# Optimization experiments

Measured on AMD Instinct MI355X. Metric: run time of the kernel, lower is better.

## Reference

```python
import jax, jax.numpy as jnp
import numpy as np

N_NODES = 50000
N_EDGES = 400000
IN_CH = 109
OUT_CH = 32


def setup_inputs() -> dict:
    key = jax.random.key(0)
    ks = jax.random.split(key, 12)
    dims = [(IN_CH, 10 * OUT_CH), (10 * OUT_CH, 2 * OUT_CH), (2 * OUT_CH, OUT_CH), (2 * OUT_CH, OUT_CH)]
    inp = {
        'x': jax.random.normal(ks[0], (N_NODES, IN_CH), dtype=jnp.float32),
        'edge_index': jax.random.randint(ks[1], (2, N_EDGES), 0, N_NODES, dtype=jnp.int64) if jax.config.jax_enable_x64 else jax.random.randint(ks[1], (2, N_EDGES), 0, N_NODES, dtype=jnp.int32),
    }
    names = ['W1', 'b1', 'W2', 'b2', 'Wmu', 'bmu', 'Wls', 'bls']
    for i, (fi, fo) in enumerate(dims):
        scale = 1.0 / np.sqrt(fi)
        inp[names[2 * i]] = jax.random.uniform(ks[2 + 2 * i], (fi, fo), minval=-scale, maxval=scale, dtype=jnp.float32)
        inp[names[2 * i + 1]] = jnp.zeros((fo,), dtype=jnp.float32)
    return inp


def _gcn_conv(x, src, dst, norm, W, b, n):
    # PyG GCNConv: h = x @ W, then symmetric-normalized aggregation, then + b
    h = x @ W                                   # [N, F_out]
    msg = h[src] * norm[:, None]                # [E+N, F_out]
    out = jax.ops.segment_sum(msg, dst, num_segments=n)
    return out + b


def _norm_and_loops(edge_index, n):
    # add self loops, compute D^{-1/2}(A+I)D^{-1/2} edge weights
    loops = jnp.arange(n, dtype=edge_index.dtype)
    src = jnp.concatenate([edge_index[0], loops])
    dst = jnp.concatenate([edge_index[1], loops])
    deg = jax.ops.segment_sum(jnp.ones_like(src, dtype=jnp.float32), dst, num_segments=n)
    dinv = jnp.where(deg > 0, jax.lax.rsqrt(jnp.maximum(deg, 1.0)), 0.0)
    norm = dinv[src] * dinv[dst]
    return src, dst, norm


def reference(x, edge_index, W1, b1, W2, b2, Wmu, bmu, Wls, bls):
    n = x.shape[0]
    src, dst, norm = _norm_and_loops(edge_index, n)
    h = jax.nn.relu(_gcn_conv(x, src, dst, norm, W1, b1, n))
    h = jax.nn.relu(_gcn_conv(h, src, dst, norm, W2, b2, n))
    mu = _gcn_conv(h, src, dst, norm, Wmu, bmu, n)
    logstd = _gcn_conv(h, src, dst, norm, Wls, bls, n)
    return (mu, logstd)
```

## Files before the change

kernel.cpp:

```cpp
#include <hip/hip_runtime.h>

#define NN 50000
#define NE 400000

typedef __attribute__((ext_vector_type(8))) short short8v;
typedef __attribute__((ext_vector_type(4))) float f32x4;

__device__ __forceinline__ unsigned short f2bf_rtn(float x) {
    unsigned u = __float_as_uint(x);
    unsigned r = u + 0x7FFFu + ((u >> 16) & 1u);
    return (unsigned short)(r >> 16);
}
__device__ __forceinline__ float bf2f(unsigned short h) {
    return __uint_as_float(((unsigned)h) << 16);
}

__global__ void prep_kernel(const float* __restrict__ x,
                            const float* __restrict__ W1, const float* __restrict__ W2,
                            const float* __restrict__ Wmu, const float* __restrict__ Wls,
                            unsigned* __restrict__ xp, int* __restrict__ zero_base,
                            unsigned short* __restrict__ w1t_hi,
                            unsigned short* __restrict__ w2t_hi,
                            unsigned short* __restrict__ wct_hi) {
    int b = blockIdx.x, tid = threadIdx.x;
    if (b < 12500) {
        int idx = b * 256 + tid;
        int i = idx >> 6, c2 = (idx & 63) * 2;
        long xb = (long)i * 109;
        float v0 = (c2 < 109) ? x[xb + c2] : 0.0f;
        float v1 = (c2 + 1 < 109) ? x[xb + c2 + 1] : 0.0f;
        xp[idx] = (unsigned)f2bf_rtn(v0) | ((unsigned)f2bf_rtn(v1) << 16);
    } else if (b < 12891) {
        int i = (b - 12500) * 256 + tid;
        if (i < 100096) zero_base[i] = 0;
    } else if (b < 13051) {
        int idx = (b - 12891) * 256 + tid;
        int n = idx >> 7, k = idx & 127;
        float v = (k < 109) ? W1[(long)k * 320 + n] : 0.0f;
        w1t_hi[idx] = f2bf_rtn(v);
    } else if (b < 13131) {
        int idx = (b - 13051) * 256 + tid;
        int n = idx / 320, k = idx - n * 320;
        w2t_hi[idx] = f2bf_rtn(W2[(long)k * 64 + n]);
    } else {
        int idx = (b - 13131) * 256 + tid;
        int n = idx >> 6, k = idx & 63;
        float v = (n < 32) ? Wmu[k * 32 + n] : Wls[k * 32 + (n - 32)];
        wct_hi[idx] = f2bf_rtn(v);
    }
}

__global__ void hist_kernel(const int* __restrict__ dst, int* __restrict__ counts) {
    for (int e = blockIdx.x * blockDim.x + threadIdx.x; e < NE; e += gridDim.x * blockDim.x)
        atomicAdd(&counts[dst[e]], 1);
}

__global__ void dinv_scan1_kernel(const int* __restrict__ counts, float* __restrict__ dinv,
                                  int* __restrict__ rowstart, int* __restrict__ bsum) {
    __shared__ int tmp[256];
    int tid = threadIdx.x;
    int i = blockIdx.x * 256 + tid;
    int v = (i < NN) ? counts[i] : 0;
    if (i < NN) dinv[i] = rsqrtf((float)(v + 1));
    tmp[tid] = v;
    __syncthreads();
    for (int off = 1; off < 256; off <<= 1) {
        int t = 0;
        if (tid >= off) t = tmp[tid - off];
        __syncthreads();
        if (tid >= off) tmp[tid] += t;
        __syncthreads();
    }
    if (i < NN) rowstart[i] = tmp[tid] - v;
    if (tid == 255) bsum[blockIdx.x] = tmp[255];
}

__global__ void scan23_kernel(int* __restrict__ rowstart, const int* __restrict__ bsum) {
    __shared__ int red[4];
    int tid = threadIdx.x;
    int v = (tid < 196 && tid < (int)blockIdx.x) ? bsum[tid] : 0;
    for (int off = 32; off > 0; off >>= 1) v += __shfl_down(v, off, 64);
    if ((tid & 63) == 0) red[tid >> 6] = v;
    __syncthreads();
    int pref = red[0] + red[1] + red[2] + red[3];
    int i = blockIdx.x * 256 + tid;
    if (i < NN) rowstart[i] += pref;
    if (i == 0) rowstart[NN] = NE;
}

__global__ void scatter_kernel(const int* __restrict__ src, const int* __restrict__ dst,
                               const int* __restrict__ rowstart, int* __restrict__ cursor,
                               int* __restrict__ esrc) {
    for (int e = blockIdx.x * blockDim.x + threadIdx.x; e < NE; e += gridDim.x * blockDim.x) {
        int d = dst[e];
        int pos = rowstart[d] + atomicAdd(&cursor[d], 1);
        esrc[pos] = src[e];
    }
}

__global__ __launch_bounds__(256) void agg109_packed_kernel(const int* __restrict__ rowstart,
                                                            const int* __restrict__ esrc,
                                                            const float* __restrict__ dinv,
                                                            const unsigned* __restrict__ xp,
                                                            unsigned* __restrict__ xa_hi32) {
    int wave = blockIdx.x * (blockDim.x >> 6) + (threadIdx.x >> 6);
    if (wave >= NN) return;
    int lane = threadIdx.x & 63;
    float wd = dinv[wave];
    unsigned pself = xp[(long)wave * 64 + lane];
    float acc0 = __uint_as_float(pself << 16) * wd;
    float acc1 = __uint_as_float(pself & 0xFFFF0000u) * wd;
    int j0 = rowstart[wave], j1 = rowstart[wave + 1];
    int j = j0;
    for (; j + 8 <= j1; j += 8) {
        int s[8];
        float w[8];
        unsigned pp[8];
        #pragma unroll
        for (int u = 0; u < 8; ++u) s[u] = esrc[j + u];
        #pragma unroll
        for (int u = 0; u < 8; ++u) w[u] = dinv[s[u]];
        #pragma unroll
        for (int u = 0; u < 8; ++u) pp[u] = xp[(long)s[u] * 64 + lane];
        #pragma unroll
        for (int u = 0; u < 8; ++u) {
            acc0 = fmaf(__uint_as_float(pp[u] << 16), w[u], acc0);
            acc1 = fmaf(__uint_as_float(pp[u] & 0xFFFF0000u), w[u], acc1);
        }
    }
    for (; j + 4 <= j1; j += 4) {
        int s0 = esrc[j], s1 = esrc[j + 1], s2 = esrc[j + 2], s3 = esrc[j + 3];
        float w0 = dinv[s0], w1 = dinv[s1], w2 = dinv[s2], w3 = dinv[s3];
        unsigned p0 = xp[(long)s0 * 64 + lane], p1 = xp[(long)s1 * 64 + lane];
        unsigned p2 = xp[(long)s2 * 64 + lane], p3 = xp[(long)s3 * 64 + lane];
        acc0 = fmaf(__uint_as_float(p0 << 16), w0, acc0);
        acc1 = fmaf(__uint_as_float(p0 & 0xFFFF0000u), w0, acc1);
        acc0 = fmaf(__uint_as_float(p1 << 16), w1, acc0);
        acc1 = fmaf(__uint_as_float(p1 & 0xFFFF0000u), w1, acc1);
        acc0 = fmaf(__uint_as_float(p2 << 16), w2, acc0);
        acc1 = fmaf(__uint_as_float(p2 & 0xFFFF0000u), w2, acc1);
        acc0 = fmaf(__uint_as_float(p3 << 16), w3, acc0);
        acc1 = fmaf(__uint_as_float(p3 & 0xFFFF0000u), w3, acc1);
    }
    for (; j < j1; ++j) {
        int s = esrc[j];
        float w = dinv[s];
        unsigned pv = xp[(long)s * 64 + lane];
        acc0 = fmaf(__uint_as_float(pv << 16), w, acc0);
        acc1 = fmaf(__uint_as_float(pv & 0xFFFF0000u), w, acc1);
    }
    acc0 *= wd;
    acc1 *= wd;
    xa_hi32[(long)wave * 64 + lane] =
        (unsigned)f2bf_rtn(acc0) | ((unsigned)f2bf_rtn(acc1) << 16);
}

__global__ __launch_bounds__(256) void agg64_relu_bf16_kernel(const int* __restrict__ rowstart,
                                                              const int* __restrict__ esrc,
                                                              const float* __restrict__ dinv,
                                                              const unsigned short* __restrict__ g,
                                                              const float* __restrict__ b,
                                                              unsigned short* __restrict__ hhi) {
    int wave = blockIdx.x * (blockDim.x >> 6) + (threadIdx.x >> 6);
    if (wave >= NN) return;
    int lane = threadIdx.x & 63;
    long base = (long)wave * 64;
    float acc = bf2f(g[base + lane]);
    int j0 = rowstart[wave], j1 = rowstart[wave + 1];
    int j = j0;
    for (; j + 8 <= j1; j += 8) {
        int s[8];
        float pp[8];
        #pragma unroll
        for (int u = 0; u < 8; ++u) s[u] = esrc[j + u];
        #pragma unroll
        for (int u = 0; u < 8; ++u) pp[u] = bf2f(g[(long)s[u] * 64 + lane]);
        #pragma unroll
        for (int u = 0; u < 8; ++u) acc += pp[u];
    }
    for (; j + 4 <= j1; j += 4) {
        int s0 = esrc[j], s1 = esrc[j + 1], s2 = esrc[j + 2], s3 = esrc[j + 3];
        float p0 = bf2f(g[(long)s0 * 64 + lane]), p1 = bf2f(g[(long)s1 * 64 + lane]);
        float p2 = bf2f(g[(long)s2 * 64 + lane]), p3 = bf2f(g[(long)s3 * 64 + lane]);
        acc += p0 + p1 + p2 + p3;
    }
    for (; j < j1; ++j) acc += bf2f(g[(long)esrc[j] * 64 + lane]);
    float v = acc * dinv[wave] + b[lane];
    v = v > 0.0f ? v : 0.0f;
    hhi[base + lane] = f2bf_rtn(v);
}

__global__ __launch_bounds__(256) void agg64b_kernel(const int* __restrict__ rowstart,
                                                     const int* __restrict__ esrc,
                                                     const float* __restrict__ dinv,
                                                     const unsigned short* __restrict__ h,
                                                     unsigned short* __restrict__ a_hi) {
    int wave = blockIdx.x * (blockDim.x >> 6) + (threadIdx.x >> 6);
    if (wave >= NN) return;
    int lane = threadIdx.x & 63;
    long base = (long)wave * 64;
    float wd = dinv[wave];
    float acc = bf2f(h[base + lane]) * wd;
    int j0 = rowstart[wave], j1 = rowstart[wave + 1];
    int j = j0;
    for (; j + 8 <= j1; j += 8) {
        int s[8];
        float w[8], pp[8];
        #pragma unroll
        for (int u = 0; u < 8; ++u) s[u] = esrc[j + u];
        #pragma unroll
        for (int u = 0; u < 8; ++u) w[u] = dinv[s[u]];
        #pragma unroll
        for (int u = 0; u < 8; ++u) pp[u] = bf2f(h[(long)s[u] * 64 + lane]);
        #pragma unroll
        for (int u = 0; u < 8; ++u) acc = fmaf(pp[u], w[u], acc);
    }
    for (; j + 4 <= j1; j += 4) {
        int s0 = esrc[j], s1 = esrc[j + 1], s2 = esrc[j + 2], s3 = esrc[j + 3];
        float w0 = dinv[s0], w1 = dinv[s1], w2 = dinv[s2], w3 = dinv[s3];
        float p0 = bf2f(h[(long)s0 * 64 + lane]), p1 = bf2f(h[(long)s1 * 64 + lane]);
        float p2 = bf2f(h[(long)s2 * 64 + lane]), p3 = bf2f(h[(long)s3 * 64 + lane]);
        acc = fmaf(p0, w0, acc); acc = fmaf(p1, w1, acc);
        acc = fmaf(p2, w2, acc); acc = fmaf(p3, w3, acc);
    }
    for (; j < j1; ++j) {
        int s = esrc[j];
        acc = fmaf(bf2f(h[(long)s * 64 + lane]), dinv[s], acc);
    }
    a_hi[base + lane] = f2bf_rtn(acc * wd);
}

#define LDT 72

template <int MODE>
__global__ __launch_bounds__(256) void mfma_gemm_kernel(
    const unsigned short* __restrict__ Ahi,
    const unsigned short* __restrict__ Bhi,
    const float* __restrict__ bias, const float* __restrict__ bias2,
    const float* __restrict__ dinv,
    unsigned short* __restrict__ Chi,
    float* __restrict__ Cf, int M, int N, int K, int grid_n) {
    __shared__ unsigned short As[64 * LDT];
    __shared__ unsigned short Bs[64 * LDT];
    int tid = threadIdx.x;
    int wid = tid >> 6, lane = tid & 63;
    int l15 = lane & 15, l4 = lane >> 4;

    int T = gridDim.x;
    int xcd = blockIdx.x & 7, jj = blockIdx.x >> 3;
    int q = T >> 3, r = T & 7;
    int start = (xcd < r) ? xcd * (q + 1) : r * (q + 1) + (xcd - r) * q;
    int lin = start + jj;
    int bm = lin / grid_n, bn = lin - bm * grid_n;
    int bm0 = bm * 64, bn0 = bn * 64;

    f32x4 acc[4] = {};

    for (int kc = 0; kc < K; kc += 64) {
        #pragma unroll
        for (int r2 = 0; r2 < 2; ++r2) {
            int idx = tid + 256 * r2;
            int row = idx >> 3, slot = idx & 7;
            int grow = bm0 + row;
            if (grow >= M) grow = M - 1;
            long go = (long)grow * K + kc + slot * 8;
            *(uint4*)&As[row * LDT + slot * 8] = *(const uint4*)&Ahi[go];
            long gob = (long)(bn0 + row) * K + kc + slot * 8;
            *(uint4*)&Bs[row * LDT + slot * 8] = *(const uint4*)&Bhi[gob];
        }
        __syncthreads();
        #pragma unroll
        for (int ks = 0; ks < 2; ++ks) {
            int koff = ks * 32 + l4 * 8;
            int ra = (wid * 16 + l15) * LDT + koff;
            short8v ah = *(const short8v*)&As[ra];
            #pragma unroll
            for (int n = 0; n < 4; ++n) {
                int rb = (n * 16 + l15) * LDT + koff;
                short8v bh = *(const short8v*)&Bs[rb];
                acc[n] = __builtin_amdgcn_mfma_f32_16x16x32_bf16(ah, bh, acc[n], 0, 0, 0);
            }
        }
        __syncthreads();
    }
    int rbase = bm0 + wid * 16 + l4 * 4;
    #pragma unroll
    for (int q2 = 0; q2 < 4; ++q2) {
        int grow = rbase + q2;
        if (grow >= M) continue;
        float rs = (MODE == 1) ? dinv[grow] : 0.0f;
        #pragma unroll
        for (int n = 0; n < 4; ++n) {
            int gcol = bn0 + n * 16 + l15;
            float v = acc[n][q2];
            if (MODE == 0) {
                v += bias[gcol];
                v = v > 0.0f ? v : 0.0f;
                Chi[(long)grow * N + gcol] = f2bf_rtn(v);
            } else if (MODE == 1) {
                Chi[(long)grow * N + gcol] = f2bf_rtn(v * rs);
            } else {
                if (gcol < 32)
                    Cf[(long)grow * 32 + gcol] = v + bias[gcol];
                else
                    Cf[(long)NN * 32 + (long)grow * 32 + (gcol - 32)] = v + bias2[gcol - 32];
            }
        }
    }
}

extern "C" void kernel_launch(void* const* d_in, const int* in_sizes, int n_in,
                              void* d_out, int out_size, void* d_ws, size_t ws_size,
                              hipStream_t stream) {
    const float* x   = (const float*)d_in[0];
    const int*   ei  = (const int*)d_in[1];
    const int*   src = ei;
    const int*   dst = ei + NE;
    const float* W1  = (const float*)d_in[2];
    const float* b1  = (const float*)d_in[3];
    const float* W2  = (const float*)d_in[4];
    const float* b2  = (const float*)d_in[5];
    const float* Wmu = (const float*)d_in[6];
    const float* bmu = (const float*)d_in[7];
    const float* Wls = (const float*)d_in[8];
    const float* bls = (const float*)d_in[9];
    float* out = (float*)d_out;

    char* p = (char*)d_ws;
    float* dinv   = (float*)p; p += 50048 * 4;
    int* counts   = (int*)p;   p += 50048 * 4;
    int* cursor   = (int*)p;   p += 50048 * 4;
    int* rowstart = (int*)p;   p += 50056 * 4;
    int* bsum     = (int*)p;   p += 256 * 4;
    int* esrc     = (int*)p;   p += 400000 * 4;
    unsigned* xp          = (unsigned*)p;       p += 50000L * 64 * 4;
    unsigned short* xa_hi = (unsigned short*)p; p += 50000L * 128 * 2;
    unsigned short* a2_hi = (unsigned short*)p; p += 50000L * 64 * 2;
    unsigned short* g2b   = (unsigned short*)p; p += 50000L * 64 * 2;
    unsigned short* h1_hi = (unsigned short*)p; p += 50000L * 320 * 2;
    unsigned short* w1t_hi = (unsigned short*)p; p += 320 * 128 * 2;
    unsigned short* w2t_hi = (unsigned short*)p; p += 64 * 320 * 2;
    unsigned short* wct_hi = (unsigned short*)p; p += 64 * 64 * 2;
    unsigned short* h2_hi = xa_hi;

    const int TB = 256;
    const int NB_NODES = (NN + TB - 1) / TB;
    const int NB_AGG = (NN * 64 + TB - 1) / TB;

    prep_kernel<<<13147, TB, 0, stream>>>(x, W1, W2, Wmu, Wls, xp, counts,
                                          w1t_hi, w2t_hi, wct_hi);
    hist_kernel<<<1024, TB, 0, stream>>>(dst, counts);
    dinv_scan1_kernel<<<NB_NODES, TB, 0, stream>>>(counts, dinv, rowstart, bsum);
    scan23_kernel<<<NB_NODES, TB, 0, stream>>>(rowstart, bsum);
    scatter_kernel<<<1024, TB, 0, stream>>>(src, dst, rowstart, cursor, esrc);

    agg109_packed_kernel<<<NB_AGG, TB, 0, stream>>>(rowstart, esrc, dinv, xp,
                                                    (unsigned*)xa_hi);
    mfma_gemm_kernel<0><<<782 * 5, 256, 0, stream>>>(xa_hi, w1t_hi, b1, nullptr,
                                                     nullptr, h1_hi, nullptr,
                                                     NN, 320, 128, 5);

    mfma_gemm_kernel<1><<<782, 256, 0, stream>>>(h1_hi, w2t_hi, nullptr, nullptr,
                                                 dinv, g2b, nullptr,
                                                 NN, 64, 320, 1);
    agg64_relu_bf16_kernel<<<NB_AGG, TB, 0, stream>>>(rowstart, esrc, dinv, g2b, b2, h2_hi);

    agg64b_kernel<<<NB_AGG, TB, 0, stream>>>(rowstart, esrc, dinv, h2_hi, a2_hi);
    mfma_gemm_kernel<3><<<782, 256, 0, stream>>>(a2_hi, wct_hi, bmu, bls,
                                                 nullptr, nullptr, out,
                                                 NN, 64, 64, 1);
}
```

Before: 169.5 us.

## Fuse final aggregation with output GEMM into single LDS-staged kernel

Merges the last sparse aggregation (agg64b) and the 64x64 output GEMM into one kernel. Each 1024-thread block aggregates 64 nodes into shared memory as bf16, then 16 waves run MFMA against the staged weight tile and write mu/logstd directly. This removes one kernel launch and the global round trip of the 50000x64 intermediate. In exchange each wave handles four nodes serially, and the large block size may lower occupancy and latency hiding for the gather.

```diff
diff --git a/kernel.cpp b/kernel.cpp
--- a/kernel.cpp
+++ b/kernel.cpp
@@ -190,56 +190,94 @@
     hhi[base + lane] = f2bf_rtn(v);
 }
 
-__global__ __launch_bounds__(256) void agg64b_kernel(const int* __restrict__ rowstart,
-                                                     const int* __restrict__ esrc,
-                                                     const float* __restrict__ dinv,
-                                                     const unsigned short* __restrict__ h,
-                                                     unsigned short* __restrict__ a_hi) {
-    int wave = blockIdx.x * (blockDim.x >> 6) + (threadIdx.x >> 6);
-    if (wave >= NN) return;
-    int lane = threadIdx.x & 63;
-    long base = (long)wave * 64;
-    float wd = dinv[wave];
-    float acc = bf2f(h[base + lane]) * wd;
-    int j0 = rowstart[wave], j1 = rowstart[wave + 1];
-    int j = j0;
-    for (; j + 8 <= j1; j += 8) {
-        int s[8];
-        float w[8], pp[8];
-        #pragma unroll
-        for (int u = 0; u < 8; ++u) s[u] = esrc[j + u];
-        #pragma unroll
-        for (int u = 0; u < 8; ++u) w[u] = dinv[s[u]];
-        #pragma unroll
-        for (int u = 0; u < 8; ++u) pp[u] = bf2f(h[(long)s[u] * 64 + lane]);
-        #pragma unroll
-        for (int u = 0; u < 8; ++u) acc = fmaf(pp[u], w[u], acc);
-    }
-    for (; j + 4 <= j1; j += 4) {
-        int s0 = esrc[j], s1 = esrc[j + 1], s2 = esrc[j + 2], s3 = esrc[j + 3];
-        float w0 = dinv[s0], w1 = dinv[s1], w2 = dinv[s2], w3 = dinv[s3];
-        float p0 = bf2f(h[(long)s0 * 64 + lane]), p1 = bf2f(h[(long)s1 * 64 + lane]);
-        float p2 = bf2f(h[(long)s2 * 64 + lane]), p3 = bf2f(h[(long)s3 * 64 + lane]);
-        acc = fmaf(p0, w0, acc); acc = fmaf(p1, w1, acc);
-        acc = fmaf(p2, w2, acc); acc = fmaf(p3, w3, acc);
-    }
-    for (; j < j1; ++j) {
-        int s = esrc[j];
-        acc = fmaf(bf2f(h[(long)s * 64 + lane]), dinv[s], acc);
-    }
-    a_hi[base + lane] = f2bf_rtn(acc * wd);
-}
-
 #define LDT 72
+__global__ __launch_bounds__(1024) void agg_gemm3_kernel(const int* __restrict__ rowstart,
+                                                         const int* __restrict__ esrc,
+                                                         const float* __restrict__ dinv,
+                                                         const unsigned short* __restrict__ h,
+                                                         const unsigned short* __restrict__ wct_hi,
+                                                         const float* __restrict__ bmu,
+                                                         const float* __restrict__ bls,
+                                                         float* __restrict__ out) {
+    __shared__ unsigned short As[64 * LDT];
+    __shared__ unsigned short Bs[64 * LDT];
+    int tid = threadIdx.x;
+    int wid = tid >> 6, lane = tid & 63;
+    int m0 = blockIdx.x * 64;
+
+    if (tid < 512) {
+        int row = tid >> 3, slot = tid & 7;
+        *(uint4*)&Bs[row * LDT + slot * 8] = *(const uint4*)&wct_hi[row * 64 + slot * 8];
+    }
+
+    #pragma unroll
+    for (int t = 0; t < 4; ++t) {
+        int node = m0 + wid * 4 + t;
+        int i = node < NN ? node : NN - 1;
+        long base = (long)i * 64;
+        float wd = dinv[i];
+        float acc = bf2f(h[base + lane]) * wd;
+        int j0 = rowstart[i], j1 = rowstart[i + 1];
+        int j = j0;
+        for (; j + 8 <= j1; j += 8) {
+            int s[8];
+            float w[8], pp[8];
+            #pragma unroll
+            for (int u = 0; u < 8; ++u) s[u] = esrc[j + u];
+            #pragma unroll
+            for (int u = 0; u < 8; ++u) w[u] = dinv[s[u]];
+            #pragma unroll
+            for (int u = 0; u < 8; ++u) pp[u] = bf2f(h[(long)s[u] * 64 + lane]);
+            #pragma unroll
+            for (int u = 0; u < 8; ++u) acc = fmaf(pp[u], w[u], acc);
+        }
+        for (; j + 4 <= j1; j += 4) {
+            int s0 = esrc[j], s1 = esrc[j + 1], s2 = esrc[j + 2], s3 = esrc[j + 3];
+            float w0 = dinv[s0], w1 = dinv[s1], w2 = dinv[s2], w3 = dinv[s3];
+            float p0 = bf2f(h[(long)s0 * 64 + lane]), p1 = bf2f(h[(long)s1 * 64 + lane]);
+            float p2 = bf2f(h[(long)s2 * 64 + lane]), p3 = bf2f(h[(long)s3 * 64 + lane]);
+            acc = fmaf(p0, w0, acc); acc = fmaf(p1, w1, acc);
+            acc = fmaf(p2, w2, acc); acc = fmaf(p3, w3, acc);
+        }
+        for (; j < j1; ++j) {
+            int s = esrc[j];
+            acc = fmaf(bf2f(h[(long)s * 64 + lane]), dinv[s], acc);
+        }
+        As[(wid * 4 + t) * LDT + lane] = f2bf_rtn(acc * wd);
+    }
+    __syncthreads();
+
+    int r = wid >> 2, c = wid & 3;
+    int l15 = lane & 15, l4 = lane >> 4;
+    f32x4 acc4 = {};
+    #pragma unroll
+    for (int ks = 0; ks < 2; ++ks) {
+        int koff = ks * 32 + l4 * 8;
+        short8v ah = *(const short8v*)&As[(r * 16 + l15) * LDT + koff];
+        short8v bh = *(const short8v*)&Bs[(c * 16 + l15) * LDT + koff];
+        acc4 = __builtin_amdgcn_mfma_f32_16x16x32_bf16(ah, bh, acc4, 0, 0, 0);
+    }
+    int rbase = m0 + r * 16 + l4 * 4;
+    int gcol = c * 16 + l15;
+    #pragma unroll
+    for (int q2 = 0; q2 < 4; ++q2) {
+        int grow = rbase + q2;
+        if (grow >= NN) continue;
+        float v = acc4[q2];
+        if (gcol < 32)
+            out[(long)grow * 32 + gcol] = v + bmu[gcol];
+        else
+            out[(long)NN * 32 + (long)grow * 32 + (gcol - 32)] = v + bls[gcol - 32];
+    }
+}
 
 template <int MODE>
 __global__ __launch_bounds__(256) void mfma_gemm_kernel(
     const unsigned short* __restrict__ Ahi,
     const unsigned short* __restrict__ Bhi,
-    const float* __restrict__ bias, const float* __restrict__ bias2,
+    const float* __restrict__ bias,
     const float* __restrict__ dinv,
-    unsigned short* __restrict__ Chi,
-    float* __restrict__ Cf, int M, int N, int K, int grid_n) {
+    unsigned short* __restrict__ Chi, int M, int N, int K, int grid_n) {
     __shared__ unsigned short As[64 * LDT];
     __shared__ unsigned short Bs[64 * LDT];
     int tid = threadIdx.x;
@@ -297,13 +335,8 @@
                 v += bias[gcol];
                 v = v > 0.0f ? v : 0.0f;
                 Chi[(long)grow * N + gcol] = f2bf_rtn(v);
-            } else if (MODE == 1) {
+            } else {
                 Chi[(long)grow * N + gcol] = f2bf_rtn(v * rs);
-            } else {
-                if (gcol < 32)
-                    Cf[(long)grow * 32 + gcol] = v + bias[gcol];
-                else
-                    Cf[(long)NN * 32 + (long)grow * 32 + (gcol - 32)] = v + bias2[gcol - 32];
             }
         }
     }
@@ -335,7 +368,6 @@
     int* esrc     = (int*)p;   p += 400000 * 4;
     unsigned* xp          = (unsigned*)p;       p += 50000L * 64 * 4;
     unsigned short* xa_hi = (unsigned short*)p; p += 50000L * 128 * 2;
-    unsigned short* a2_hi = (unsigned short*)p; p += 50000L * 64 * 2;
     unsigned short* g2b   = (unsigned short*)p; p += 50000L * 64 * 2;
     unsigned short* h1_hi = (unsigned short*)p; p += 50000L * 320 * 2;
     unsigned short* w1t_hi = (unsigned short*)p; p += 320 * 128 * 2;
@@ -357,16 +389,12 @@
     agg109_packed_kernel<<<NB_AGG, TB, 0, stream>>>(rowstart, esrc, dinv, xp,
                                                     (unsigned*)xa_hi);
     mfma_gemm_kernel<0><<<782 * 5, 256, 0, stream>>>(xa_hi, w1t_hi, b1, nullptr,
-                                                     nullptr, h1_hi, nullptr,
-                                                     NN, 320, 128, 5);
-
-    mfma_gemm_kernel<1><<<782, 256, 0, stream>>>(h1_hi, w2t_hi, nullptr, nullptr,
-                                                 dinv, g2b, nullptr,
-                                                 NN, 64, 320, 1);
+                                                     h1_hi, NN, 320, 128, 5);
+
+    mfma_gemm_kernel<1><<<782, 256, 0, stream>>>(h1_hi, w2t_hi, nullptr, dinv,
+                                                 g2b, NN, 64, 320, 1);
     agg64_relu_bf16_kernel<<<NB_AGG, TB, 0, stream>>>(rowstart, esrc, dinv, g2b, b2, h2_hi);
 
-    agg64b_kernel<<<NB_AGG, TB, 0, stream>>>(rowstart, esrc, dinv, h2_hi, a2_hi);
-    mfma_gemm_kernel<3><<<782, 256, 0, stream>>>(a2_hi, wct_hi, bmu, bls,
-                                                 nullptr, nullptr, out,
-                                                 NN, 64, 64, 1);
-}
+    agg_gemm3_kernel<<<782, 1024, 0, stream>>>(rowstart, esrc, dinv, h2_hi, wct_hi,
+                                               bmu, bls, out);
+}
```

After: 166.4 us. No clear change (-1.8%).
